# Performance work log

Measured on AMD Instinct MI355X. Metric: run time of the kernel, lower is better.

## Reference

```python
import jax, jax.numpy as jnp
import numpy as np


def setup_inputs() -> dict:
    key = jax.random.key(0)
    k1, k2, k3 = jax.random.split(key, 3)
    B, F, K = 16384, 512, 1000
    D = jax.random.normal(k1, (B, F), dtype=jnp.float32)
    weight = jax.random.normal(k2, (K, F), dtype=jnp.float32)  # (out_features, in_features)
    gamma = jax.random.uniform(k3, (K,), dtype=jnp.float32)
    return {"D": D, "weight": weight, "gamma": gamma}


def reference(D, weight, gamma):
    # Squared Euclidean distance from each row of D to each centroid (row of weight),
    # computed via ||a||^2 + ||b||^2 - 2 a.b (mathematically equal to the broadcast
    # subtract-square-sum in the original torch forward with d_view=None).
    d_sq = jnp.sum(D * D, axis=1, keepdims=True)            # (B, 1)
    w_sq = jnp.sum(weight * weight, axis=1)                  # (K,)
    cross = jnp.einsum('bf,kf->bk', D, weight)               # (B, K)
    dist_sq = d_sq + w_sq[None, :] - 2.0 * cross             # (B, K)
    return -dist_sq * gamma                                  # (B, K)
```

## Files before the change

### kernel.cpp

```cpp
#include <hip/hip_runtime.h>
#include <hip/hip_bf16.h>
#include <stdint.h>

#define B_ROWS 16384
#define F_DIM  512
#define K_OUT  1000
#define K_PAD  1024

#define BM 128
#define BN 128
#define BK 64

typedef __attribute__((ext_vector_type(4))) float f32x4;
typedef __attribute__((ext_vector_type(8))) short short8;
typedef unsigned short u16;
typedef unsigned int   u32;

#define OFF_DB   0
#define OFF_WB   16777216
#define OFF_DSQ  (16777216 + 1048576)
#define OFF_WSQ  (16777216 + 1048576 + 65536)

__device__ __forceinline__ u16 f2bf(float f) {
  union { float f; u32 u; } v; v.f = f;
  u32 u = v.u;
  u32 r = (u + 0x7fffu + ((u >> 16) & 1u)) >> 16;
  return (u16)r;
}

__global__ void prep(const float* __restrict__ D, const float* __restrict__ W,
                     u16* __restrict__ Db, u16* __restrict__ Wb,
                     float* __restrict__ dsq, float* __restrict__ wsq) {
  int w    = threadIdx.x >> 6;
  int lane = threadIdx.x & 63;
  if (blockIdx.x < B_ROWS / 4) {
    int row = blockIdx.x * 4 + w;
    const float* src = D + (size_t)row * F_DIM + lane * 8;
    float4 v0 = *(const float4*)src;
    float4 v1 = *(const float4*)(src + 4);
    float s = v0.x*v0.x + v0.y*v0.y + v0.z*v0.z + v0.w*v0.w
            + v1.x*v1.x + v1.y*v1.y + v1.z*v1.z + v1.w*v1.w;
#pragma unroll
    for (int off = 32; off >= 1; off >>= 1) s += __shfl_xor(s, off);
    if (lane == 0) dsq[row] = s;
    uint4 p;
    p.x = (u32)f2bf(v0.x) | ((u32)f2bf(v0.y) << 16);
    p.y = (u32)f2bf(v0.z) | ((u32)f2bf(v0.w) << 16);
    p.z = (u32)f2bf(v1.x) | ((u32)f2bf(v1.y) << 16);
    p.w = (u32)f2bf(v1.z) | ((u32)f2bf(v1.w) << 16);
    *(uint4*)(Db + (size_t)row * F_DIM + lane * 8) = p;
  } else {
    int row = (blockIdx.x - B_ROWS / 4) * 4 + w;
    uint4 p; p.x = p.y = p.z = p.w = 0u;
    float s = 0.f;
    if (row < K_OUT) {
      const float* src = W + (size_t)row * F_DIM + lane * 8;
      float4 v0 = *(const float4*)src;
      float4 v1 = *(const float4*)(src + 4);
      s = v0.x*v0.x + v0.y*v0.y + v0.z*v0.z + v0.w*v0.w
        + v1.x*v1.x + v1.y*v1.y + v1.z*v1.z + v1.w*v1.w;
      p.x = (u32)f2bf(v0.x) | ((u32)f2bf(v0.y) << 16);
      p.y = (u32)f2bf(v0.z) | ((u32)f2bf(v0.w) << 16);
      p.z = (u32)f2bf(v1.x) | ((u32)f2bf(v1.y) << 16);
      p.w = (u32)f2bf(v1.z) | ((u32)f2bf(v1.w) << 16);
    }
#pragma unroll
    for (int off = 32; off >= 1; off >>= 1) s += __shfl_xor(s, off);
    if (lane == 0) wsq[row] = s;
    *(uint4*)(Wb + (size_t)row * F_DIM + lane * 8) = p;
  }
}

__device__ __forceinline__ void gload_lds16(const void* g, void* l) {
  __builtin_amdgcn_global_load_lds(
      (const __attribute__((address_space(1))) void*)g,
      (__attribute__((address_space(3))) void*)l,
      16, 0, 0);
}


#define STAGE_A(h)                                                             \
  _Pragma("unroll") for (int j = 0; j < 2; ++j) {                              \
    int rb = (h) * 32 + j * 64 + w * 8;                                        \
    int r  = rb + (lane >> 3);                                                 \
    int sc = s8 ^ (r & 7);                                                     \
    gload_lds16(Ag + (size_t)r * F_DIM + kbn + sc * 8, sAn + rb * 128);        \
  }

#define STAGE_B(q)                                                             \
  _Pragma("unroll") for (int j = 0; j < 2; ++j) {                              \
    int rb = (q) * 32 + j * 64 + w * 8;                                        \
    int r  = rb + (lane >> 3);                                                 \
    int sc = s8 ^ (r & 7);                                                     \
    gload_lds16(Bg + (size_t)r * F_DIM + kbn + sc * 8, sBn + rb * 128);        \
  }

__global__ __launch_bounds__(256, 2) void gemm_eps(
    const u16* __restrict__ A,
    const u16* __restrict__ Bw,
    const float* __restrict__ dsq,
    const float* __restrict__ wsq,
    const float* __restrict__ gamma,
    float* __restrict__ out) {
  __shared__ __align__(16) char lds[65536];

  const int tid  = threadIdx.x;
  const int w    = tid >> 6;
  const int lane = tid & 63;
  const int lr   = lane & 15;
  const int lk4  = lane >> 4;
  const int wm   = w >> 1;
  const int wn   = w & 1;

  const int bid = blockIdx.x;
  const int wg  = (bid & 7) * 128 + (bid >> 3);
  const int mt  = wg >> 3;
  const int nt  = wg & 7;
  const int m0  = mt * BM;
  const int n0  = nt * BN;

  const u16* Ag = A  + (size_t)m0 * F_DIM;
  const u16* Bg = Bw + (size_t)n0 * F_DIM;

  const int s8 = lane & 7;

  f32x4 acc[4][4];
#pragma unroll
  for (int i = 0; i < 4; ++i)
#pragma unroll
    for (int j = 0; j < 4; ++j) acc[i][j] = (f32x4){0.f, 0.f, 0.f, 0.f};

  float g_[4], wq_[4];
  float4 dl[4];
#pragma unroll
  for (int ni = 0; ni < 4; ++ni) {
    int col = n0 + wn * 64 + ni * 16 + lr;
    g_[ni]  = (col < K_OUT) ? gamma[col] : 0.f;
    wq_[ni] = wsq[col & (K_PAD - 1)];
  }
#pragma unroll
  for (int mi = 0; mi < 4; ++mi)
    dl[mi] = *(const float4*)&dsq[m0 + wm * 64 + mi * 16 + lk4 * 4];

  {
    char* sAn = lds;
    char* sBn = lds + 16384;
    const int kbn = 0;
    STAGE_A(0) STAGE_A(1) STAGE_B(0) STAGE_B(1)
  }

#pragma unroll 2
  for (int t = 0; t < 8; ++t) {
    char* sAc = lds + (t & 1) * 32768;
    char* sBc = sAc + 16384;
    char* sAn = lds + ((t + 1) & 1) * 32768;
    char* sBn = sAn + 16384;
    const int kbn = ((t + 1) & 7) * BK;

    STAGE_A(0) STAGE_A(1) STAGE_B(0) STAGE_B(1)

    asm volatile("s_waitcnt vmcnt(8)" ::: "memory");
    __builtin_amdgcn_s_barrier();
    asm volatile("" ::: "memory");

    short8 a[2][4], b[2][4];
#pragma unroll
    for (int kk = 0; kk < 2; ++kk)
#pragma unroll
      for (int mi = 0; mi < 4; ++mi) {
        int rA = wm * 64 + mi * 16 + lr;
        a[kk][mi] = *(const short8*)(sAc + rA * 128 +
                                     ((((kk << 2) + lk4) ^ (rA & 7)) << 4));
        int rB = wn * 64 + mi * 16 + lr;
        b[kk][mi] = *(const short8*)(sBc + rB * 128 +
                                     ((((kk << 2) + lk4) ^ (rB & 7)) << 4));
      }

    __builtin_amdgcn_s_setprio(1);
#pragma unroll
    for (int kk = 0; kk < 2; ++kk)
#pragma unroll
      for (int mi = 0; mi < 4; ++mi)
#pragma unroll
        for (int ni = 0; ni < 4; ++ni)
          acc[mi][ni] = __builtin_amdgcn_mfma_f32_16x16x32_bf16(
              a[kk][mi], b[kk][ni], acc[mi][ni], 0, 0, 0);
    __builtin_amdgcn_s_setprio(0);

    asm volatile("" ::: "memory");
    __builtin_amdgcn_s_barrier();
  }

  float* ch = (float*)lds;
  const int rl = tid >> 3;
  const int cb = (tid & 7) << 2;
#pragma unroll
  for (int c = 0; c < 2; ++c) {
    __syncthreads();
    if (wm == c) {
#pragma unroll
      for (int mi = 0; mi < 4; ++mi) {
        const int row_l = mi * 16 + lk4 * 4;
#pragma unroll
        for (int j = 0; j < 4; ++j) {
          float dq = (j == 0) ? dl[mi].x : (j == 1) ? dl[mi].y
                   : (j == 2) ? dl[mi].z : dl[mi].w;
#pragma unroll
          for (int ni = 0; ni < 4; ++ni) {
            ch[(row_l + j) * 132 + wn * 64 + ni * 16 + lr] =
                g_[ni] * (2.f * acc[mi][ni][j] - dq - wq_[ni]);
          }
        }
      }
    }
    __syncthreads();
#pragma unroll
    for (int half = 0; half < 2; ++half) {
#pragma unroll
      for (int s = 0; s < 4; ++s) {
        int row = half * 32 + rl;
        int col = cb + s * 32;
        if (n0 + col < K_OUT) {
          float4 v = *(const float4*)&ch[row * 132 + col];
          *(float4*)&out[(size_t)(m0 + c * 64 + row) * K_OUT + n0 + col] = v;
        }
      }
    }
  }
}

extern "C" void kernel_launch(void* const* d_in, const int* in_sizes, int n_in,
                              void* d_out, int out_size, void* d_ws, size_t ws_size,
                              hipStream_t stream) {
  const float* D     = (const float*)d_in[0];
  const float* W     = (const float*)d_in[1];
  const float* gamma = (const float*)d_in[2];
  float* out = (float*)d_out;
  char*  ws  = (char*)d_ws;

  u16*   Db  = (u16*)(ws + OFF_DB);
  u16*   Wb  = (u16*)(ws + OFF_WB);
  float* dsq = (float*)(ws + OFF_DSQ);
  float* wsq = (float*)(ws + OFF_WSQ);

  prep<<<B_ROWS / 4 + K_PAD / 4, 256, 0, stream>>>(D, W, Db, Wb, dsq, wsq);

  gemm_eps<<<(B_ROWS / BM) * (K_PAD / BN), 256, 0, stream>>>(
      Db, Wb, dsq, wsq, gamma, out);
}
```

Baseline: 39.73 us.

## Halve K-tile to BK=32 to fit four workgroups per CU

Reduces the K tile from 64 to 32, halving LDS use to about 33 KB so launch bounds can request four blocks per CU instead of two. The staging macros, swizzle and fragment loads are rewritten for 64-byte rows, and the loop now runs 16 iterations. The epilogue scalar loads (gamma, wsq, dsq) move after the main loop to shorten register live ranges. The cost is twice as many barriers and waits per tile, with less MFMA work between each sync, and the 4-block bound may force register spilling with 64 accumulator floats per thread.

```diff
diff --git a/kernel.cpp b/kernel.cpp
--- a/kernel.cpp
+++ b/kernel.cpp
@@ -9,7 +9,7 @@
 
 #define BM 128
 #define BN 128
-#define BK 64
+#define BK 32
 
 typedef __attribute__((ext_vector_type(4))) float f32x4;
 typedef __attribute__((ext_vector_type(8))) short short8;
@@ -79,30 +79,30 @@
 }
 
 
-#define STAGE_A(h)                                                             \
-  _Pragma("unroll") for (int j = 0; j < 2; ++j) {                              \
-    int rb = (h) * 32 + j * 64 + w * 8;                                        \
-    int r  = rb + (lane >> 3);                                                 \
-    int sc = s8 ^ (r & 7);                                                     \
-    gload_lds16(Ag + (size_t)r * F_DIM + kbn + sc * 8, sAn + rb * 128);        \
-  }
-
-#define STAGE_B(q)                                                             \
-  _Pragma("unroll") for (int j = 0; j < 2; ++j) {                              \
-    int rb = (q) * 32 + j * 64 + w * 8;                                        \
-    int r  = rb + (lane >> 3);                                                 \
-    int sc = s8 ^ (r & 7);                                                     \
-    gload_lds16(Bg + (size_t)r * F_DIM + kbn + sc * 8, sBn + rb * 128);        \
-  }
-
-__global__ __launch_bounds__(256, 2) void gemm_eps(
+#define STAGE_A(j)                                                             \
+  {                                                                            \
+    int rb = (j) * 64 + w * 16;                                                \
+    int r  = rb + (lane >> 2);                                                 \
+    int sc = (lane & 3) ^ (r & 3);                                             \
+    gload_lds16(Ag + (size_t)r * F_DIM + kbn + sc * 8, sAn + rb * 64);         \
+  }
+
+#define STAGE_B(j)                                                             \
+  {                                                                            \
+    int rb = (j) * 64 + w * 16;                                                \
+    int r  = rb + (lane >> 2);                                                 \
+    int sc = (lane & 3) ^ (r & 3);                                             \
+    gload_lds16(Bg + (size_t)r * F_DIM + kbn + sc * 8, sBn + rb * 64);         \
+  }
+
+__global__ __launch_bounds__(256, 4) void gemm_eps(
     const u16* __restrict__ A,
     const u16* __restrict__ Bw,
     const float* __restrict__ dsq,
     const float* __restrict__ wsq,
     const float* __restrict__ gamma,
     float* __restrict__ out) {
-  __shared__ __align__(16) char lds[65536];
+  __shared__ __align__(16) char lds[33792];
 
   const int tid  = threadIdx.x;
   const int w    = tid >> 6;
@@ -122,13 +122,54 @@
   const u16* Ag = A  + (size_t)m0 * F_DIM;
   const u16* Bg = Bw + (size_t)n0 * F_DIM;
 
-  const int s8 = lane & 7;
-
   f32x4 acc[4][4];
 #pragma unroll
   for (int i = 0; i < 4; ++i)
 #pragma unroll
     for (int j = 0; j < 4; ++j) acc[i][j] = (f32x4){0.f, 0.f, 0.f, 0.f};
+
+  {
+    char* sAn = lds;
+    char* sBn = lds + 8192;
+    const int kbn = 0;
+    STAGE_A(0) STAGE_A(1) STAGE_B(0) STAGE_B(1)
+  }
+
+#pragma unroll 2
+  for (int t = 0; t < 16; ++t) {
+    char* sAc = lds + (t & 1) * 16384;
+    char* sBc = sAc + 8192;
+    char* sAn = lds + ((t + 1) & 1) * 16384;
+    char* sBn = sAn + 8192;
+    const int kbn = ((t + 1) & 15) * BK;
+
+    STAGE_A(0) STAGE_A(1) STAGE_B(0) STAGE_B(1)
+
+    asm volatile("s_waitcnt vmcnt(4)" ::: "memory");
+    __builtin_amdgcn_s_barrier();
+    asm volatile("" ::: "memory");
+
+    short8 a[4], b[4];
+#pragma unroll
+    for (int mi = 0; mi < 4; ++mi) {
+      int rA = wm * 64 + mi * 16 + lr;
+      a[mi] = *(const short8*)(sAc + rA * 64 + ((lk4 ^ (rA & 3)) << 4));
+      int rB = wn * 64 + mi * 16 + lr;
+      b[mi] = *(const short8*)(sBc + rB * 64 + ((lk4 ^ (rB & 3)) << 4));
+    }
+
+    __builtin_amdgcn_s_setprio(1);
+#pragma unroll
+    for (int mi = 0; mi < 4; ++mi)
+#pragma unroll
+      for (int ni = 0; ni < 4; ++ni)
+        acc[mi][ni] = __builtin_amdgcn_mfma_f32_16x16x32_bf16(
+            a[mi], b[ni], acc[mi][ni], 0, 0, 0);
+    __builtin_amdgcn_s_setprio(0);
+
+    asm volatile("" ::: "memory");
+    __builtin_amdgcn_s_barrier();
+  }
 
   float g_[4], wq_[4];
   float4 dl[4];
@@ -141,55 +182,6 @@
 #pragma unroll
   for (int mi = 0; mi < 4; ++mi)
     dl[mi] = *(const float4*)&dsq[m0 + wm * 64 + mi * 16 + lk4 * 4];
-
-  {
-    char* sAn = lds;
-    char* sBn = lds + 16384;
-    const int kbn = 0;
-    STAGE_A(0) STAGE_A(1) STAGE_B(0) STAGE_B(1)
-  }
-
-#pragma unroll 2
-  for (int t = 0; t < 8; ++t) {
-    char* sAc = lds + (t & 1) * 32768;
-    char* sBc = sAc + 16384;
-    char* sAn = lds + ((t + 1) & 1) * 32768;
-    char* sBn = sAn + 16384;
-    const int kbn = ((t + 1) & 7) * BK;
-
-    STAGE_A(0) STAGE_A(1) STAGE_B(0) STAGE_B(1)
-
-    asm volatile("s_waitcnt vmcnt(8)" ::: "memory");
-    __builtin_amdgcn_s_barrier();
-    asm volatile("" ::: "memory");
-
-    short8 a[2][4], b[2][4];
-#pragma unroll
-    for (int kk = 0; kk < 2; ++kk)
-#pragma unroll
-      for (int mi = 0; mi < 4; ++mi) {
-        int rA = wm * 64 + mi * 16 + lr;
-        a[kk][mi] = *(const short8*)(sAc + rA * 128 +
-                                     ((((kk << 2) + lk4) ^ (rA & 7)) << 4));
-        int rB = wn * 64 + mi * 16 + lr;
-        b[kk][mi] = *(const short8*)(sBc + rB * 128 +
-                                     ((((kk << 2) + lk4) ^ (rB & 7)) << 4));
-      }
-
-    __builtin_amdgcn_s_setprio(1);
-#pragma unroll
-    for (int kk = 0; kk < 2; ++kk)
-#pragma unroll
-      for (int mi = 0; mi < 4; ++mi)
-#pragma unroll
-        for (int ni = 0; ni < 4; ++ni)
-          acc[mi][ni] = __builtin_amdgcn_mfma_f32_16x16x32_bf16(
-              a[kk][mi], b[kk][ni], acc[mi][ni], 0, 0, 0);
-    __builtin_amdgcn_s_setprio(0);
-
-    asm volatile("" ::: "memory");
-    __builtin_amdgcn_s_barrier();
-  }
 
   float* ch = (float*)lds;
   const int rl = tid >> 3;
```

After: 42.47 us. 6.9% more time.

## Shrink GEMM N-tile to 64 and raise occupancy to three blocks per CU

Applied to the files above, without the earlier changes.

Halves the block tile width from 128 to 64 columns, so each wave computes a 64x32 sub-tile with a 4x2 accumulator array. This shrinks LDS to 48KB and the register footprint, and launch bounds now request three blocks per CU. The staging loads, waitcnt, block-id swizzle and epilogue are rewritten to match. The goal is more waves in flight and more blocks to fill the CUs, at the cost of lower arithmetic intensity per block and more reloading of the A tile from global memory or L2.

```diff
diff --git a/kernel.cpp b/kernel.cpp
--- a/kernel.cpp
+++ b/kernel.cpp
@@ -8,7 +8,7 @@
 #define K_PAD  1024
 
 #define BM 128
-#define BN 128
+#define BN 64
 #define BK 64
 
 typedef __attribute__((ext_vector_type(4))) float f32x4;
@@ -20,6 +20,12 @@
 #define OFF_WB   16777216
 #define OFF_DSQ  (16777216 + 1048576)
 #define OFF_WSQ  (16777216 + 1048576 + 65536)
+
+#define A0_OFF   0
+#define A1_OFF   16384
+#define B0_OFF   32768
+#define B1_OFF   40960
+#define LDS_SZ   49152
 
 __device__ __forceinline__ u16 f2bf(float f) {
   union { float f; u32 u; } v; v.f = f;
@@ -79,30 +85,30 @@
 }
 
 
-#define STAGE_A(h)                                                             \
-  _Pragma("unroll") for (int j = 0; j < 2; ++j) {                              \
-    int rb = (h) * 32 + j * 64 + w * 8;                                        \
-    int r  = rb + (lane >> 3);                                                 \
-    int sc = s8 ^ (r & 7);                                                     \
-    gload_lds16(Ag + (size_t)r * F_DIM + kbn + sc * 8, sAn + rb * 128);        \
-  }
-
-#define STAGE_B(q)                                                             \
-  _Pragma("unroll") for (int j = 0; j < 2; ++j) {                              \
-    int rb = (q) * 32 + j * 64 + w * 8;                                        \
-    int r  = rb + (lane >> 3);                                                 \
-    int sc = s8 ^ (r & 7);                                                     \
-    gload_lds16(Bg + (size_t)r * F_DIM + kbn + sc * 8, sBn + rb * 128);        \
-  }
-
-__global__ __launch_bounds__(256, 2) void gemm_eps(
+#define STAGE_A(i)                                                             \
+  {                                                                            \
+    int r  = (i) * 32 + (tid >> 3);                                            \
+    int sc = (tid & 7) ^ (r & 7);                                              \
+    gload_lds16(Ag + (size_t)r * F_DIM + kbn + sc * 8,                         \
+                sAn + (i) * 4096 + w * 1024);                                  \
+  }
+
+#define STAGE_B(j)                                                             \
+  {                                                                            \
+    int r  = (j) * 32 + (tid >> 3);                                            \
+    int sc = (tid & 7) ^ (r & 7);                                              \
+    gload_lds16(Bg + (size_t)r * F_DIM + kbn + sc * 8,                         \
+                sBn + (j) * 4096 + w * 1024);                                  \
+  }
+
+__global__ __launch_bounds__(256, 3) void gemm_eps(
     const u16* __restrict__ A,
     const u16* __restrict__ Bw,
     const float* __restrict__ dsq,
     const float* __restrict__ wsq,
     const float* __restrict__ gamma,
     float* __restrict__ out) {
-  __shared__ __align__(16) char lds[65536];
+  __shared__ __align__(16) char lds[LDS_SZ];
 
   const int tid  = threadIdx.x;
   const int w    = tid >> 6;
@@ -113,28 +119,26 @@
   const int wn   = w & 1;
 
   const int bid = blockIdx.x;
-  const int wg  = (bid & 7) * 128 + (bid >> 3);
-  const int mt  = wg >> 3;
-  const int nt  = wg & 7;
+  const int wg  = (bid & 7) * 256 + (bid >> 3);
+  const int mt  = wg >> 4;
+  const int nt  = wg & 15;
   const int m0  = mt * BM;
   const int n0  = nt * BN;
 
   const u16* Ag = A  + (size_t)m0 * F_DIM;
   const u16* Bg = Bw + (size_t)n0 * F_DIM;
 
-  const int s8 = lane & 7;
-
-  f32x4 acc[4][4];
+  f32x4 acc[4][2];
 #pragma unroll
   for (int i = 0; i < 4; ++i)
 #pragma unroll
-    for (int j = 0; j < 4; ++j) acc[i][j] = (f32x4){0.f, 0.f, 0.f, 0.f};
-
-  float g_[4], wq_[4];
+    for (int j = 0; j < 2; ++j) acc[i][j] = (f32x4){0.f, 0.f, 0.f, 0.f};
+
+  float g_[2], wq_[2];
   float4 dl[4];
 #pragma unroll
-  for (int ni = 0; ni < 4; ++ni) {
-    int col = n0 + wn * 64 + ni * 16 + lr;
+  for (int ni = 0; ni < 2; ++ni) {
+    int col = n0 + wn * 32 + ni * 16 + lr;
     g_[ni]  = (col < K_OUT) ? gamma[col] : 0.f;
     wq_[ni] = wsq[col & (K_PAD - 1)];
   }
@@ -143,38 +147,44 @@
     dl[mi] = *(const float4*)&dsq[m0 + wm * 64 + mi * 16 + lk4 * 4];
 
   {
-    char* sAn = lds;
-    char* sBn = lds + 16384;
+    char* sAn = lds + A0_OFF;
+    char* sBn = lds + B0_OFF;
     const int kbn = 0;
-    STAGE_A(0) STAGE_A(1) STAGE_B(0) STAGE_B(1)
+    STAGE_A(0) STAGE_A(1) STAGE_A(2) STAGE_A(3)
+    STAGE_B(0) STAGE_B(1)
   }
 
 #pragma unroll 2
   for (int t = 0; t < 8; ++t) {
-    char* sAc = lds + (t & 1) * 32768;
-    char* sBc = sAc + 16384;
-    char* sAn = lds + ((t + 1) & 1) * 32768;
-    char* sBn = sAn + 16384;
+    const char* sAc = lds + ((t & 1) ? A1_OFF : A0_OFF);
+    const char* sBc = lds + ((t & 1) ? B1_OFF : B0_OFF);
+    char* sAn = lds + ((t & 1) ? A0_OFF : A1_OFF);
+    char* sBn = lds + ((t & 1) ? B0_OFF : B1_OFF);
     const int kbn = ((t + 1) & 7) * BK;
 
-    STAGE_A(0) STAGE_A(1) STAGE_B(0) STAGE_B(1)
-
-    asm volatile("s_waitcnt vmcnt(8)" ::: "memory");
+    STAGE_A(0) STAGE_A(1) STAGE_A(2) STAGE_A(3)
+    STAGE_B(0) STAGE_B(1)
+
+    asm volatile("s_waitcnt vmcnt(6)" ::: "memory");
     __builtin_amdgcn_s_barrier();
     asm volatile("" ::: "memory");
 
-    short8 a[2][4], b[2][4];
-#pragma unroll
-    for (int kk = 0; kk < 2; ++kk)
+    short8 a[2][4], b[2][2];
+#pragma unroll
+    for (int kk = 0; kk < 2; ++kk) {
 #pragma unroll
       for (int mi = 0; mi < 4; ++mi) {
         int rA = wm * 64 + mi * 16 + lr;
         a[kk][mi] = *(const short8*)(sAc + rA * 128 +
                                      ((((kk << 2) + lk4) ^ (rA & 7)) << 4));
-        int rB = wn * 64 + mi * 16 + lr;
-        b[kk][mi] = *(const short8*)(sBc + rB * 128 +
+      }
+#pragma unroll
+      for (int ni = 0; ni < 2; ++ni) {
+        int rB = wn * 32 + ni * 16 + lr;
+        b[kk][ni] = *(const short8*)(sBc + rB * 128 +
                                      ((((kk << 2) + lk4) ^ (rB & 7)) << 4));
       }
+    }
 
     __builtin_amdgcn_s_setprio(1);
 #pragma unroll
@@ -182,7 +192,7 @@
 #pragma unroll
       for (int mi = 0; mi < 4; ++mi)
 #pragma unroll
-        for (int ni = 0; ni < 4; ++ni)
+        for (int ni = 0; ni < 2; ++ni)
           acc[mi][ni] = __builtin_amdgcn_mfma_f32_16x16x32_bf16(
               a[kk][mi], b[kk][ni], acc[mi][ni], 0, 0, 0);
     __builtin_amdgcn_s_setprio(0);
@@ -192,8 +202,8 @@
   }
 
   float* ch = (float*)lds;
-  const int rl = tid >> 3;
-  const int cb = (tid & 7) << 2;
+  const int rl = tid >> 2;
+  const int cb = (tid & 3) << 2;
 #pragma unroll
   for (int c = 0; c < 2; ++c) {
     __syncthreads();
@@ -206,8 +216,8 @@
           float dq = (j == 0) ? dl[mi].x : (j == 1) ? dl[mi].y
                    : (j == 2) ? dl[mi].z : dl[mi].w;
 #pragma unroll
-          for (int ni = 0; ni < 4; ++ni) {
-            ch[(row_l + j) * 132 + wn * 64 + ni * 16 + lr] =
+          for (int ni = 0; ni < 2; ++ni) {
+            ch[(row_l + j) * 68 + wn * 32 + ni * 16 + lr] =
                 g_[ni] * (2.f * acc[mi][ni][j] - dq - wq_[ni]);
           }
         }
@@ -215,15 +225,11 @@
     }
     __syncthreads();
 #pragma unroll
-    for (int half = 0; half < 2; ++half) {
-#pragma unroll
-      for (int s = 0; s < 4; ++s) {
-        int row = half * 32 + rl;
-        int col = cb + s * 32;
-        if (n0 + col < K_OUT) {
-          float4 v = *(const float4*)&ch[row * 132 + col];
-          *(float4*)&out[(size_t)(m0 + c * 64 + row) * K_OUT + n0 + col] = v;
-        }
+    for (int s = 0; s < 4; ++s) {
+      int col = cb + s * 16;
+      if (n0 + col < K_OUT) {
+        float4 v = *(const float4*)&ch[rl * 68 + col];
+        *(float4*)&out[(size_t)(m0 + c * 64 + rl) * K_OUT + n0 + col] = v;
       }
     }
   }
```

Result: slower. 42.18 us (+6.2%).
